# Kernel optimization log

Measured on AMD Instinct MI355X. Metric: run time of the kernel, lower is better.

The kernel has to match this reference:

```python
import jax, jax.numpy as jnp
import numpy as np

NUM_HEADS = 12
HIDDEN = 768
HEAD_DIM = HIDDEN // NUM_HEADS
SCALE = HEAD_DIM ** -0.5


def setup_inputs() -> dict:
    key = jax.random.key(0)
    k1, k2, k3 = jax.random.split(key, 3)
    b, n = 2, 2048
    x = jax.random.normal(k1, (b, n, HIDDEN), dtype=jnp.float32)
    w_qkv = jax.random.normal(k2, (3 * HIDDEN, HIDDEN), dtype=jnp.float32) * (HIDDEN ** -0.5)
    w_out = jax.random.normal(k3, (HIDDEN, HIDDEN), dtype=jnp.float32) * (HIDDEN ** -0.5)
    b_out = jnp.zeros((HIDDEN,), dtype=jnp.float32)
    return {"x": x, "w_qkv": w_qkv, "w_out": w_out, "b_out": b_out}


def reference(x, w_qkv, w_out, b_out):
    b, n, h = x.shape  # [b, seq, hidden]
    # qkv linear (no bias), then 'b n (qkv heads d) -> qkv b heads n d'
    qkv = (x @ w_qkv.T).reshape(b, n, 3, NUM_HEADS, HEAD_DIM)
    qkv = qkv.transpose(2, 0, 3, 1, 4)
    q, k, v = qkv[0], qkv[1], qkv[2]  # each [b, heads, n, d]
    att = jax.nn.softmax(jnp.einsum('bhxd,bhyd->bhxy', q, k) * SCALE, axis=-1)
    out = jnp.einsum('bhxy,bhyd->bhxd', att, v)
    out = out.transpose(0, 2, 1, 3).reshape(b, n, h)  # 'b h n d -> b n (h d)'
    return out @ w_out.T + b_out
```

## Files before the change

### kernel.cpp

```cpp
#include <hip/hip_runtime.h>
#include <hip/hip_bf16.h>
#include <cstdint>
#include <cstddef>

#define SEQ    2048
#define BATCH  2
#define HID    768
#define NH     12
#define HD     64
#define QKV_N  2304

typedef __attribute__((ext_vector_type(8))) short bf16x8;
typedef __attribute__((ext_vector_type(4))) float f32x4;
typedef __attribute__((ext_vector_type(16))) float f32x16;

#define AS1C(p) ((const __attribute__((address_space(1))) void*)(p))
#define AS3(p)  ((__attribute__((address_space(3))) void*)(p))

static __device__ __forceinline__ short f2bf(float x) {
  __hip_bfloat16 h = __float2bfloat16(x);
  short s;
  __builtin_memcpy(&s, &h, 2);
  return s;
}
static __device__ __forceinline__ float bf2f(short s) {
  __hip_bfloat16 h;
  __builtin_memcpy(&h, &s, 2);
  return __bfloat162float(h);
}
static __device__ __forceinline__ float fast_exp2(float x) {
  return __builtin_amdgcn_exp2f(x);
}

__global__ __launch_bounds__(256)
void cvt3_f32_bf16(const float* __restrict__ s0, short* __restrict__ d0,
                   const float* __restrict__ s1, short* __restrict__ d1,
                   const float* __restrict__ s2, short* __restrict__ d2) {
  int bid = blockIdx.x;
  const float* src;
  short* dst;
  if (bid < 1536)      { src = s0; dst = d0; }
  else if (bid < 2400) { src = s1; dst = d1; bid -= 1536; }
  else                 { src = s2; dst = d2; bid -= 2400; }
  const int i = (bid * 256 + threadIdx.x) * 8;
  const float4 a = *reinterpret_cast<const float4*>(src + i);
  const float4 b = *reinterpret_cast<const float4*>(src + i + 4);
  bf16x8 o;
  o[0] = f2bf(a.x); o[1] = f2bf(a.y); o[2] = f2bf(a.z); o[3] = f2bf(a.w);
  o[4] = f2bf(b.x); o[5] = f2bf(b.y); o[6] = f2bf(b.z); o[7] = f2bf(b.w);
  *reinterpret_cast<bf16x8*>(dst + i) = o;
}

template <bool BF16_OUT>
__global__ __launch_bounds__(256)
void gemm_nt_mfma(const short* __restrict__ A, const short* __restrict__ B,
                  const float* __restrict__ bias,
                  float* __restrict__ Cf, short* __restrict__ Cb,
                  int M, int N, int K) {
  __shared__ short As[128][64];
  __shared__ short Bs[128][64];

  const int t = threadIdx.x;
  const int w = t >> 6;
  const int l = t & 63;
  const int g = l >> 4;
  const int n = l & 15;

  const int m0 = blockIdx.y * 128;
  const int n0 = blockIdx.x * 128;
  const int wr = (w >> 1) * 64;
  const int wc = (w & 1) * 64;

  const int srow = w * 32 + (l >> 3);
  const int scol = (l & 7) * 8;
  const short* Ag = A + (size_t)(m0 + srow) * K + scol;
  const short* Bg = B + (size_t)(n0 + srow) * K + scol;

  f32x4 acc[4][4] = {};

  for (int k0 = 0; k0 < K; k0 += 64) {
    __syncthreads();
#pragma unroll
    for (int it = 0; it < 4; ++it) {
      __builtin_amdgcn_global_load_lds(AS1C(Ag + (size_t)(it * 8) * K + k0),
                                       AS3(&As[w * 32 + it * 8][0]), 16, 0, 0);
    }
#pragma unroll
    for (int it = 0; it < 4; ++it) {
      __builtin_amdgcn_global_load_lds(AS1C(Bg + (size_t)(it * 8) * K + k0),
                                       AS3(&Bs[w * 32 + it * 8][0]), 16, 0, 0);
    }
    __syncthreads();

#pragma unroll
    for (int kk = 0; kk < 2; ++kk) {
      bf16x8 af[4], bfr[4];
#pragma unroll
      for (int m = 0; m < 4; ++m)
        af[m] = *reinterpret_cast<const bf16x8*>(&As[wr + m * 16 + n][kk * 32 + g * 8]);
#pragma unroll
      for (int j = 0; j < 4; ++j)
        bfr[j] = *reinterpret_cast<const bf16x8*>(&Bs[wc + j * 16 + n][kk * 32 + g * 8]);
#pragma unroll
      for (int m = 0; m < 4; ++m)
#pragma unroll
        for (int j = 0; j < 4; ++j)
          acc[m][j] = __builtin_amdgcn_mfma_f32_16x16x32_bf16(af[m], bfr[j], acc[m][j], 0, 0, 0);
    }
  }

#pragma unroll
  for (int m = 0; m < 4; ++m) {
#pragma unroll
    for (int r = 0; r < 4; ++r) {
      const size_t row = m0 + wr + m * 16 + g * 4 + r;
#pragma unroll
      for (int j = 0; j < 4; ++j) {
        const int col = n0 + wc + j * 16 + n;
        float v = acc[m][j][r];
        if (bias) v += bias[col];
        if (BF16_OUT) Cb[row * N + col] = f2bf(v);
        else          Cf[row * N + col] = v;
      }
    }
  }
}

__global__ __launch_bounds__(256)
void gemm_nt_mfma64(const short* __restrict__ A, const short* __restrict__ B,
                    const float* __restrict__ bias, float* __restrict__ Cf,
                    int M, int N, int K) {
  __shared__ short As[64][64];
  __shared__ short Bs[64][64];

  const int t = threadIdx.x;
  const int w = t >> 6;
  const int l = t & 63;
  const int g = l >> 4;
  const int n = l & 15;

  const int m0 = blockIdx.y * 64;
  const int n0 = blockIdx.x * 64;
  const int wr = (w >> 1) * 32;
  const int wc = (w & 1) * 32;

  const int srow = t >> 3;
  const int scol = (t & 7) * 8;
  const short* Ag = A + (size_t)(m0 + srow) * K + scol;
  const short* Bg = B + (size_t)(n0 + srow) * K + scol;

  f32x4 acc[2][2] = {};

  for (int k0 = 0; k0 < K; k0 += 64) {
    __syncthreads();
#pragma unroll
    for (int it = 0; it < 2; ++it) {
      __builtin_amdgcn_global_load_lds(AS1C(Ag + (size_t)(it * 32) * K + k0),
                                       AS3(&As[w * 8 + it * 32][0]), 16, 0, 0);
    }
#pragma unroll
    for (int it = 0; it < 2; ++it) {
      __builtin_amdgcn_global_load_lds(AS1C(Bg + (size_t)(it * 32) * K + k0),
                                       AS3(&Bs[w * 8 + it * 32][0]), 16, 0, 0);
    }
    __syncthreads();

#pragma unroll
    for (int kk = 0; kk < 2; ++kk) {
      bf16x8 af[2], bfr[2];
#pragma unroll
      for (int m = 0; m < 2; ++m)
        af[m] = *reinterpret_cast<const bf16x8*>(&As[wr + m * 16 + n][kk * 32 + g * 8]);
#pragma unroll
      for (int j = 0; j < 2; ++j)
        bfr[j] = *reinterpret_cast<const bf16x8*>(&Bs[wc + j * 16 + n][kk * 32 + g * 8]);
#pragma unroll
      for (int m = 0; m < 2; ++m)
#pragma unroll
        for (int j = 0; j < 2; ++j)
          acc[m][j] = __builtin_amdgcn_mfma_f32_16x16x32_bf16(af[m], bfr[j], acc[m][j], 0, 0, 0);
    }
  }

#pragma unroll
  for (int m = 0; m < 2; ++m) {
#pragma unroll
    for (int r = 0; r < 4; ++r) {
      const size_t row = m0 + wr + m * 16 + g * 4 + r;
#pragma unroll
      for (int j = 0; j < 2; ++j) {
        const int col = n0 + wc + j * 16 + n;
        Cf[row * N + col] = acc[m][j][r] + bias[col];
      }
    }
  }
}

__global__ __launch_bounds__(256)
void transpose_v(const short* __restrict__ qkv, short* __restrict__ vtg) {
  const int bh  = blockIdx.x;
  const int kvt = blockIdx.y;
  const int b   = bh / NH;
  const int h   = bh % NH;

  __shared__ short Lt[64][72];

  const int t  = threadIdx.x;
  const int ry = t >> 2;
  const int rd = (t & 3) * 16;

  const short* src = qkv + (size_t)(b * SEQ + kvt * 64 + ry) * QKV_N
                         + 2 * HID + h * HD + rd;
  bf16x8 a0 = *reinterpret_cast<const bf16x8*>(src);
  bf16x8 a1 = *reinterpret_cast<const bf16x8*>(src + 8);
  *reinterpret_cast<bf16x8*>(&Lt[ry][rd])     = a0;
  *reinterpret_cast<bf16x8*>(&Lt[ry][rd + 8]) = a1;
  __syncthreads();

  const int wd = t >> 2;
  const int wy = (t & 3) * 16;
  bf16x8 o0, o1;
#pragma unroll
  for (int j = 0; j < 8; ++j) {
    o0[j] = Lt[wy + j][wd];
    o1[j] = Lt[wy + 8 + j][wd];
  }
  short* dst = vtg + ((size_t)bh * 64 + wd) * SEQ + kvt * 64 + wy;
  *reinterpret_cast<bf16x8*>(dst)     = o0;
  *reinterpret_cast<bf16x8*>(dst + 8) = o1;
}

__global__ __launch_bounds__(512)
void attn_mfma(const short* __restrict__ qkv, const short* __restrict__ vtg,
               short* __restrict__ att) {
  const int bh = blockIdx.x;
  const int qt = blockIdx.y;
  const int b  = bh / NH;
  const int h0 = bh % NH;
  const int q0 = qt * 64;

  const int t   = threadIdx.x;
  const int w   = t >> 6;
  const int l   = t & 63;
  const int hi  = l >> 5;
  const int q31 = l & 31;
  const int qq  = w >> 2;
  const int kh  = w & 3;

  __shared__ __align__(16) char smem[53248];
  short* KxL = (short*)smem;
  short* VxL = (short*)(smem + 16384);
  short* PsL = (short*)(smem + 32768);

  const short* baseq = qkv + (size_t)b * SEQ * QKV_N + h0 * HD;
  const short* Kg    = baseq + HID;
  const short* vt_bh = vtg + (size_t)bh * 64 * SEQ;

  bf16x8 qf[4];
  {
    const short* qrow = baseq + (size_t)(q0 + qq * 32 + q31) * QKV_N;
#pragma unroll
    for (int c16 = 0; c16 < 4; ++c16) {
      bf16x8 raw = *reinterpret_cast<const bf16x8*>(qrow + c16 * 16 + hi * 8);
#pragma unroll
      for (int j = 0; j < 8; ++j)
        qf[c16][j] = f2bf(bf2f(raw[j]) * 0.1803368801f);
    }
  }

  f32x16 o0 = {};
  f32x16 o1 = {};
  float mrow = -3e38f;
  float lrow = 0.f;

  const int kv0  = t >> 3;
  const int dg0  = (t & 7) ^ (kv0 & 7);
  const int kv1  = kv0 + 64;
  const int dg1  = (t & 7) ^ (kv1 & 7);
  const short* ks0 = Kg + (size_t)kv0 * QKV_N + dg0 * 8;
  const short* ks1 = Kg + (size_t)kv1 * QKV_N + dg1 * 8;

  const int vd0  = t >> 4;
  const int vd1  = vd0 + 32;
  const short* vls0 = vt_bh + (size_t)vd0 * SEQ + (t & 15) * 8;
  const short* vls1 = vt_bh + (size_t)vd1 * SEQ + (t & 15) * 8;
  short* vwd0 = VxL + vd0 * 128 + (((t & 15) ^ (vd0 & 15)) * 8);
  short* vwd1 = VxL + vd1 * 128 + (((t & 15) ^ (vd1 & 15)) * 8);
  const short* vs0 = vt_bh + (size_t)vd0 * SEQ + (((t & 15) ^ (vd0 & 15)) * 8);
  const short* vs1 = vt_bh + (size_t)vd1 * SEQ + (((t & 15) ^ (vd1 & 15)) * 8);

  __builtin_amdgcn_global_load_lds(AS1C(ks0), AS3(KxL + w * 512), 16, 0, 0);
  __builtin_amdgcn_global_load_lds(AS1C(ks1), AS3(KxL + w * 512 + 4096), 16, 0, 0);
  __builtin_amdgcn_global_load_lds(AS1C(vs0), AS3(VxL + w * 512), 16, 0, 0);
  __builtin_amdgcn_global_load_lds(AS1C(vs1), AS3(VxL + w * 512 + 4096), 16, 0, 0);
  __syncthreads();

  const int krow = kh * 32 + q31;
  const int kxor = l & 7;
  const int vx0  = q31 & 15;

  for (int ti = 0; ti < SEQ / 128; ++ti) {
    const bool have_next = (ti + 1) < SEQ / 128;

    f32x16 sc = {};
#pragma unroll
    for (int c16 = 0; c16 < 4; ++c16) {
      bf16x8 kb = *reinterpret_cast<const bf16x8*>(
          (const char*)KxL + krow * 128 + (((c16 * 2 + hi) ^ kxor) << 4));
      sc = __builtin_amdgcn_mfma_f32_32x32x16_bf16(kb, qf[c16], sc, 0, 0, 0);
    }
    __syncthreads();

    bf16x8 vA, vB;
    if (have_next) {
      const size_t rb = (size_t)(ti + 1) * 128 * QKV_N;
      __builtin_amdgcn_global_load_lds(AS1C(ks0 + rb), AS3(KxL + w * 512), 16, 0, 0);
      __builtin_amdgcn_global_load_lds(AS1C(ks1 + rb), AS3(KxL + w * 512 + 4096), 16, 0, 0);
      const size_t vb = (size_t)(ti + 1) * 128;
      vA = *reinterpret_cast<const bf16x8*>(vls0 + vb);
      vB = *reinterpret_cast<const bf16x8*>(vls1 + vb);
    }

    {
      float pm = fmaxf(fmaxf(sc[0], sc[1]), fmaxf(sc[2], sc[3]));
#pragma unroll
      for (int r = 4; r < 16; r += 4)
        pm = fmaxf(pm, fmaxf(fmaxf(sc[r], sc[r + 1]), fmaxf(sc[r + 2], sc[r + 3])));
      pm = fmaxf(pm, __shfl_xor(pm, 32));
      if (__any(pm - mrow > 8.f)) {
        const float mnew = fmaxf(mrow, pm);
        const float corr = fast_exp2(mrow - mnew);
        mrow = mnew;
        lrow *= corr;
#pragma unroll
        for (int r = 0; r < 16; ++r) { o0[r] *= corr; o1[r] *= corr; }
      }
      float psum = 0.f;
#pragma unroll
      for (int rr = 0; rr < 4; ++rr) {
        const float p0 = fast_exp2(sc[rr * 4 + 0] - mrow);
        const float p1 = fast_exp2(sc[rr * 4 + 1] - mrow);
        const float p2 = fast_exp2(sc[rr * 4 + 2] - mrow);
        const float p3 = fast_exp2(sc[rr * 4 + 3] - mrow);
        psum += (p0 + p1) + (p2 + p3);
        short4 pk;
        pk.x = f2bf(p0); pk.y = f2bf(p1); pk.z = f2bf(p2); pk.w = f2bf(p3);
        *reinterpret_cast<short4*>(
            &PsL[w * 1280 + q31 * 40 + rr * 8 + hi * 4]) = pk;
      }
      lrow += psum;
    }

#pragma unroll
    for (int c = 0; c < 2; ++c) {
      bf16x8 pb = *reinterpret_cast<const bf16x8*>(
          &PsL[w * 1280 + q31 * 40 + c * 16 + hi * 8]);
      const int kvg = kh * 4 + c * 2 + hi;
      {
        bf16x8 va = *reinterpret_cast<const bf16x8*>(
            (const char*)VxL + q31 * 256 + ((kvg ^ vx0) << 4));
        o0 = __builtin_amdgcn_mfma_f32_32x32x16_bf16(va, pb, o0, 0, 0, 0);
      }
      {
        bf16x8 va = *reinterpret_cast<const bf16x8*>(
            (const char*)VxL + (32 + q31) * 256 + ((kvg ^ vx0) << 4));
        o1 = __builtin_amdgcn_mfma_f32_32x32x16_bf16(va, pb, o1, 0, 0, 0);
      }
    }
    __syncthreads();

    if (have_next) {
      *reinterpret_cast<bf16x8*>(vwd0) = vA;
      *reinterpret_cast<bf16x8*>(vwd1) = vB;
    }
  }

  lrow += __shfl_xor(lrow, 32);

  float* mbf = (float*)smem;
  const int base = (qq * 2 + (kh >> 1)) * 2176 + l * 34;
  if (kh & 1) {
#pragma unroll
    for (int r = 0; r < 16; ++r) { mbf[base + r] = o0[r]; mbf[base + 16 + r] = o1[r]; }
    mbf[base + 32] = mrow;
    mbf[base + 33] = lrow;
  }
  __syncthreads();
  if (!(kh & 1)) {
    const float m2 = mbf[base + 32];
    const float l2 = mbf[base + 33];
    const float mn = fmaxf(mrow, m2);
    const float ca = fast_exp2(mrow - mn);
    const float cb = fast_exp2(m2 - mn);
#pragma unroll
    for (int r = 0; r < 16; ++r) {
      o0[r] = o0[r] * ca + mbf[base + r] * cb;
      o1[r] = o1[r] * ca + mbf[base + 16 + r] * cb;
    }
    lrow = lrow * ca + l2 * cb;
    mrow = mn;
  }
  __syncthreads();
  const int base2 = qq * 2176 + l * 34;
  if (kh == 2) {
#pragma unroll
    for (int r = 0; r < 16; ++r) { mbf[base2 + r] = o0[r]; mbf[base2 + 16 + r] = o1[r]; }
    mbf[base2 + 32] = mrow;
    mbf[base2 + 33] = lrow;
  }
  __syncthreads();
  if (kh == 0) {
    const float m2 = mbf[base2 + 32];
    const float l2 = mbf[base2 + 33];
    const float mn = fmaxf(mrow, m2);
    const float ca = fast_exp2(mrow - mn);
    const float cb = fast_exp2(m2 - mn);
    const float lm = lrow * ca + l2 * cb;
    const float linv = 1.f / lm;
    short* orow = att + (size_t)(b * SEQ + q0 + qq * 32 + q31) * HID + h0 * HD;
#pragma unroll
    for (int rr = 0; rr < 4; ++rr) {
      short4 ov;
      ov.x = f2bf((o0[rr * 4 + 0] * ca + mbf[base2 + rr * 4 + 0] * cb) * linv);
      ov.y = f2bf((o0[rr * 4 + 1] * ca + mbf[base2 + rr * 4 + 1] * cb) * linv);
      ov.z = f2bf((o0[rr * 4 + 2] * ca + mbf[base2 + rr * 4 + 2] * cb) * linv);
      ov.w = f2bf((o0[rr * 4 + 3] * ca + mbf[base2 + rr * 4 + 3] * cb) * linv);
      *reinterpret_cast<short4*>(&orow[rr * 8 + hi * 4]) = ov;
      short4 ow;
      ow.x = f2bf((o1[rr * 4 + 0] * ca + mbf[base2 + 16 + rr * 4 + 0] * cb) * linv);
      ow.y = f2bf((o1[rr * 4 + 1] * ca + mbf[base2 + 16 + rr * 4 + 1] * cb) * linv);
      ow.z = f2bf((o1[rr * 4 + 2] * ca + mbf[base2 + 16 + rr * 4 + 2] * cb) * linv);
      ow.w = f2bf((o1[rr * 4 + 3] * ca + mbf[base2 + 16 + rr * 4 + 3] * cb) * linv);
      *reinterpret_cast<short4*>(&orow[32 + rr * 8 + hi * 4]) = ow;
    }
  }
}

extern "C" void kernel_launch(void* const* d_in, const int* in_sizes, int n_in,
                              void* d_out, int out_size, void* d_ws, size_t ws_size,
                              hipStream_t stream) {
  const float* x     = (const float*)d_in[0];
  const float* w_qkv = (const float*)d_in[1];
  const float* w_out = (const float*)d_in[2];
  const float* b_out = (const float*)d_in[3];
  float* out = (float*)d_out;

  const int NX  = BATCH * SEQ * HID;
  const int NWQ = QKV_N * HID;
  const int NWO = HID * HID;

  char* ws = (char*)d_ws;
  short* xb   = (short*)ws;  ws += (size_t)NX  * 2;
  short* wqb  = (short*)ws;  ws += (size_t)NWQ * 2;
  short* wob  = (short*)ws;  ws += (size_t)NWO * 2;
  short* qkvb = (short*)ws;  ws += (size_t)BATCH * SEQ * QKV_N * 2;
  short* attb = (short*)ws;  ws += (size_t)BATCH * SEQ * HID * 2;
  short* vtg  = (short*)ws;

  cvt3_f32_bf16<<<dim3(2688), dim3(256), 0, stream>>>(x, xb, w_qkv, wqb, w_out, wob);

  gemm_nt_mfma<true><<<dim3(QKV_N / 128, (BATCH * SEQ) / 128), dim3(256), 0, stream>>>(
      xb, wqb, nullptr, nullptr, qkvb, BATCH * SEQ, QKV_N, HID);

  transpose_v<<<dim3(BATCH * NH, SEQ / 64), dim3(256), 0, stream>>>(qkvb, vtg);

  attn_mfma<<<dim3(BATCH * NH, SEQ / 64), dim3(512), 0, stream>>>(qkvb, vtg, attb);

  gemm_nt_mfma64<<<dim3(HID / 64, (BATCH * SEQ) / 64), dim3(256), 0, stream>>>(
      attb, wob, b_out, out, BATCH * SEQ, HID, HID);
}
```

Measured before the change: 111.1 us.

## Fuse V transpose into QKV GEMM epilogue and retile to 128x96

The QKV projection GEMM now writes the V columns directly in transposed [b,h,d,seq] layout from its epilogue, which removes the separate transpose_v kernel launch and its extra read and write of V. The N tile shrinks from 128 to 96 so that each block lies entirely within the Q/K or the V region (1536 divides by 96) and the grid grows to 24x32 blocks for better CU coverage. In exchange the transposed stores are 8-byte short4 writes strided by SEQ, less coalesced than before, and each MFMA tile gets less reuse of the A operand.

```diff
diff --git a/kernel.cpp b/kernel.cpp
--- a/kernel.cpp
+++ b/kernel.cpp
@@ -51,14 +51,12 @@
   *reinterpret_cast<bf16x8*>(dst + i) = o;
 }
 
-template <bool BF16_OUT>
 __global__ __launch_bounds__(256)
-void gemm_nt_mfma(const short* __restrict__ A, const short* __restrict__ B,
-                  const float* __restrict__ bias,
-                  float* __restrict__ Cf, short* __restrict__ Cb,
-                  int M, int N, int K) {
+void gemm_qkv(const short* __restrict__ A, const short* __restrict__ B,
+              short* __restrict__ C, short* __restrict__ vtg) {
+  const int K = HID, N = QKV_N;
   __shared__ short As[128][64];
-  __shared__ short Bs[128][64];
+  __shared__ short Bs[96][64];
 
   const int t = threadIdx.x;
   const int w = t >> 6;
@@ -67,16 +65,17 @@
   const int n = l & 15;
 
   const int m0 = blockIdx.y * 128;
-  const int n0 = blockIdx.x * 128;
+  const int n0 = blockIdx.x * 96;
   const int wr = (w >> 1) * 64;
-  const int wc = (w & 1) * 64;
-
-  const int srow = w * 32 + (l >> 3);
-  const int scol = (l & 7) * 8;
-  const short* Ag = A + (size_t)(m0 + srow) * K + scol;
-  const short* Bg = B + (size_t)(n0 + srow) * K + scol;
-
-  f32x4 acc[4][4] = {};
+  const int wc = (w & 1) * 48;
+
+  const int srowA = w * 32 + (l >> 3);
+  const int srowB = w * 24 + (l >> 3);
+  const int scol  = (l & 7) * 8;
+  const short* Ag = A + (size_t)(m0 + srowA) * K + scol;
+  const short* Bg = B + (size_t)(n0 + srowB) * K + scol;
+
+  f32x4 acc[4][3] = {};
 
   for (int k0 = 0; k0 < K; k0 += 64) {
     __syncthreads();
@@ -86,41 +85,59 @@
                                        AS3(&As[w * 32 + it * 8][0]), 16, 0, 0);
     }
 #pragma unroll
-    for (int it = 0; it < 4; ++it) {
+    for (int it = 0; it < 3; ++it) {
       __builtin_amdgcn_global_load_lds(AS1C(Bg + (size_t)(it * 8) * K + k0),
-                                       AS3(&Bs[w * 32 + it * 8][0]), 16, 0, 0);
+                                       AS3(&Bs[w * 24 + it * 8][0]), 16, 0, 0);
     }
     __syncthreads();
 
 #pragma unroll
     for (int kk = 0; kk < 2; ++kk) {
-      bf16x8 af[4], bfr[4];
+      bf16x8 af[4], bfr[3];
 #pragma unroll
       for (int m = 0; m < 4; ++m)
         af[m] = *reinterpret_cast<const bf16x8*>(&As[wr + m * 16 + n][kk * 32 + g * 8]);
 #pragma unroll
-      for (int j = 0; j < 4; ++j)
+      for (int j = 0; j < 3; ++j)
         bfr[j] = *reinterpret_cast<const bf16x8*>(&Bs[wc + j * 16 + n][kk * 32 + g * 8]);
 #pragma unroll
       for (int m = 0; m < 4; ++m)
 #pragma unroll
-        for (int j = 0; j < 4; ++j)
+        for (int j = 0; j < 3; ++j)
           acc[m][j] = __builtin_amdgcn_mfma_f32_16x16x32_bf16(af[m], bfr[j], acc[m][j], 0, 0, 0);
     }
   }
 
-#pragma unroll
-  for (int m = 0; m < 4; ++m) {
-#pragma unroll
-    for (int r = 0; r < 4; ++r) {
-      const size_t row = m0 + wr + m * 16 + g * 4 + r;
-#pragma unroll
-      for (int j = 0; j < 4; ++j) {
-        const int col = n0 + wc + j * 16 + n;
-        float v = acc[m][j][r];
-        if (bias) v += bias[col];
-        if (BF16_OUT) Cb[row * N + col] = f2bf(v);
-        else          Cf[row * N + col] = v;
+  if (n0 < 1536) {
+#pragma unroll
+    for (int m = 0; m < 4; ++m) {
+#pragma unroll
+      for (int r = 0; r < 4; ++r) {
+        const size_t row = m0 + wr + m * 16 + g * 4 + r;
+#pragma unroll
+        for (int j = 0; j < 3; ++j) {
+          const int col = n0 + wc + j * 16 + n;
+          C[row * N + col] = f2bf(acc[m][j][r]);
+        }
+      }
+    }
+  } else {
+    const int b = m0 >> 11;
+#pragma unroll
+    for (int m = 0; m < 4; ++m) {
+      const int kvbase = (m0 & 2047) + wr + m * 16 + g * 4;
+#pragma unroll
+      for (int j = 0; j < 3; ++j) {
+        const int col2 = n0 - 1536 + wc + j * 16 + n;
+        const int h = col2 >> 6;
+        const int d = col2 & 63;
+        short4 pk;
+        pk.x = f2bf(acc[m][j][0]);
+        pk.y = f2bf(acc[m][j][1]);
+        pk.z = f2bf(acc[m][j][2]);
+        pk.w = f2bf(acc[m][j][3]);
+        *reinterpret_cast<short4*>(
+            &vtg[(((size_t)b * NH + h) * 64 + d) * SEQ + kvbase]) = pk;
       }
     }
   }
@@ -194,40 +211,6 @@
       }
     }
   }
-}
-
-__global__ __launch_bounds__(256)
-void transpose_v(const short* __restrict__ qkv, short* __restrict__ vtg) {
-  const int bh  = blockIdx.x;
-  const int kvt = blockIdx.y;
-  const int b   = bh / NH;
-  const int h   = bh % NH;
-
-  __shared__ short Lt[64][72];
-
-  const int t  = threadIdx.x;
-  const int ry = t >> 2;
-  const int rd = (t & 3) * 16;
-
-  const short* src = qkv + (size_t)(b * SEQ + kvt * 64 + ry) * QKV_N
-                         + 2 * HID + h * HD + rd;
-  bf16x8 a0 = *reinterpret_cast<const bf16x8*>(src);
-  bf16x8 a1 = *reinterpret_cast<const bf16x8*>(src + 8);
-  *reinterpret_cast<bf16x8*>(&Lt[ry][rd])     = a0;
-  *reinterpret_cast<bf16x8*>(&Lt[ry][rd + 8]) = a1;
-  __syncthreads();
-
-  const int wd = t >> 2;
-  const int wy = (t & 3) * 16;
-  bf16x8 o0, o1;
-#pragma unroll
-  for (int j = 0; j < 8; ++j) {
-    o0[j] = Lt[wy + j][wd];
-    o1[j] = Lt[wy + 8 + j][wd];
-  }
-  short* dst = vtg + ((size_t)bh * 64 + wd) * SEQ + kvt * 64 + wy;
-  *reinterpret_cast<bf16x8*>(dst)     = o0;
-  *reinterpret_cast<bf16x8*>(dst + 8) = o1;
 }
 
 __global__ __launch_bounds__(512)
@@ -459,10 +442,8 @@
 
   cvt3_f32_bf16<<<dim3(2688), dim3(256), 0, stream>>>(x, xb, w_qkv, wqb, w_out, wob);
 
-  gemm_nt_mfma<true><<<dim3(QKV_N / 128, (BATCH * SEQ) / 128), dim3(256), 0, stream>>>(
-      xb, wqb, nullptr, nullptr, qkvb, BATCH * SEQ, QKV_N, HID);
-
-  transpose_v<<<dim3(BATCH * NH, SEQ / 64), dim3(256), 0, stream>>>(qkvb, vtg);
+  gemm_qkv<<<dim3(QKV_N / 96, (BATCH * SEQ) / 128), dim3(256), 0, stream>>>(
+      xb, wqb, qkvb, vtg);
 
   attn_mfma<<<dim3(BATCH * NH, SEQ / 64), dim3(512), 0, stream>>>(qkvb, vtg, attb);
 
```

New measurement: 92.40 us (median of 5 runs). 1.2x faster.
